# Performance work log

Measured on AMD Instinct MI355X. Metric: run time of the kernel, lower is better.

Reference implementation:

```python
import jax, jax.numpy as jnp
import numpy as np

NUM_CLASSES = 80
MASK_SIZE = 3
ATTRIBS = 5 + NUM_CLASSES
NET_W = 608.0
NET_H = 608.0
# Faithful to the original indexing bug: anchor_w = masked_anchors[a], anchor_h = masked_anchors[a+1]
MASKED_ANCHORS = np.array([10.0, 13.0, 16.0, 30.0, 33.0, 23.0], dtype=np.float32)
ANCHOR_W = jnp.asarray(MASKED_ANCHORS[0:MASK_SIZE])      # [10, 13, 16]
ANCHOR_H = jnp.asarray(MASKED_ANCHORS[1:MASK_SIZE + 1])  # [13, 16, 30]


def setup_inputs() -> dict:
    key = jax.random.key(0)
    x = jax.random.normal(key, (16, MASK_SIZE * ATTRIBS, 76, 76), dtype=jnp.float32)
    return {"x": x}


def reference(x):
    B, C, H, W = x.shape
    # (B, A, attribs, H, W) -> (B, A, H, W, attribs)
    pred = x.reshape(B, MASK_SIZE, ATTRIBS, H, W).transpose(0, 1, 3, 4, 2)
    tx = jax.nn.sigmoid(pred[..., 0])
    ty = jax.nn.sigmoid(pred[..., 1])
    tw = pred[..., 2]
    th = pred[..., 3]
    conf = jax.nn.sigmoid(pred[..., 4])
    pred_cls = jax.nn.sigmoid(pred[..., 5:])

    gi = jnp.arange(W, dtype=x.dtype)[None, None, None, :]  # column index i
    gj = jnp.arange(H, dtype=x.dtype)[None, None, :, None]  # row index j
    bx = (gi + tx) / W
    by = (gj + ty) / H
    bw = jnp.exp(tw) * ANCHOR_W[None, :, None, None] / NET_W
    bh = jnp.exp(th) * ANCHOR_H[None, :, None, None] / NET_H

    boxes = jnp.stack([bx, by, bw, bh], axis=-1)  # (B, A, H, W, 4)
    # (B, A, H, W, 4+1+num_classes)
    return jnp.concatenate([boxes, conf[..., None], pred_cls], axis=-1)
```

## Files before the change

### kernel.cpp

```cpp
#include <hip/hip_runtime.h>
#include <stdint.h>

#define NB      16
#define NA      3
#define HH_     76
#define WW_     76
#define S_TOT   (HH_ * WW_)
#define ATTR    85
#define TILE_S  76
#define TILES   (S_TOT / TILE_S)
#define CHUNKS4 (TILE_S / 4)
#define UNITS_L (ATTR * CHUNKS4)
#define UNITS_S (TILE_S * ATTR / 4)
#define NTHREADS 256
#define LOG2E   1.44269504088896340f

typedef __attribute__((ext_vector_type(4))) float float4v;

__device__ __forceinline__ float fast_sigmoid(float x) {
    float e = __builtin_amdgcn_exp2f(x * (-LOG2E));
    return __builtin_amdgcn_rcpf(1.0f + e);
}

__global__ __launch_bounds__(NTHREADS)
void yolo_layer_kernel(const float* __restrict__ in,
                       float* __restrict__ out) {
    __shared__ __attribute__((aligned(16))) float lds[TILE_S * ATTR];

    const int tid  = threadIdx.x;
    const int tile = blockIdx.x;
    const int BA   = blockIdx.y;
    const int a    = BA % NA;
    const int s0   = tile * TILE_S;

    const float aw = (a == 0) ? 10.0f : (a == 1) ? 13.0f : 16.0f;
    const float ah = (a == 0) ? 13.0f : (a == 1) ? 16.0f : 30.0f;
    const float cw = aw * (1.0f / 608.0f);
    const float ch = ah * (1.0f / 608.0f);

    const float* inb = in + (size_t)BA * (ATTR * S_TOT) + s0;

    for (int u = tid; u < UNITS_L; u += NTHREADS) {
        const int k  = u / CHUNKS4;
        const int c  = u - k * CHUNKS4;
        const int sl = c * 4;

        const float4v v = *(const float4v*)(inb + (size_t)k * S_TOT + sl);
        float r[4];

        if (k >= 4) {
            #pragma unroll
            for (int j = 0; j < 4; ++j) {
                r[j] = fast_sigmoid(v[j]);
            }
        } else {
            #pragma unroll
            for (int j = 0; j < 4; ++j) {
                float x  = v[j];
                int   sp = s0 + sl + j;
                int   hy = sp / WW_;
                int   wx = sp - hy * WW_;
                if      (k == 0) r[j] = ((float)wx + fast_sigmoid(x)) * (1.0f / 76.0f);
                else if (k == 1) r[j] = ((float)hy + fast_sigmoid(x)) * (1.0f / 76.0f);
                else if (k == 2) r[j] = __builtin_amdgcn_exp2f(x * LOG2E) * cw;
                else             r[j] = __builtin_amdgcn_exp2f(x * LOG2E) * ch;
            }
        }

        float* lp = &lds[sl * ATTR + k];
        #pragma unroll
        for (int j = 0; j < 4; ++j) {
            lp[j * ATTR] = r[j];
        }
    }

    __syncthreads();

    float4v* outv = (float4v*)(out + ((size_t)BA * S_TOT + s0) * ATTR);
    const float4v* ldsv = (const float4v*)lds;
    for (int u = tid; u < UNITS_S; u += NTHREADS) {
        outv[u] = ldsv[u];
    }
}

extern "C" void kernel_launch(void* const* d_in, const int* in_sizes, int n_in,
                              void* d_out, int out_size, void* d_ws, size_t ws_size,
                              hipStream_t stream) {
    const float* in = (const float*)d_in[0];
    float* out = (float*)d_out;

    dim3 grid(TILES, NB * NA);
    dim3 block(NTHREADS);
    yolo_layer_kernel<<<grid, block, 0, stream>>>(in, out);
}
```

Baseline: 168.8 us.

## Give each wave a private 16-position tile with all loads issued upfront

Each wavefront now owns its own 16-position spatial micro-tile and its own LDS slice. The block-wide __syncthreads is gone, and the grid becomes one-dimensional over all micro-tiles. Every lane issues six float4 loads before doing any math, which raises memory-level parallelism, and output goes out through nontemporal stores with a launch-bounds occupancy hint. The cost is shorter contiguous input reads (64 bytes per attribute row instead of 304). A few lanes also do redundant clamped loads and rewrite the same values to the last attribute row.

```diff
diff --git a/kernel.cpp b/kernel.cpp
--- a/kernel.cpp
+++ b/kernel.cpp
@@ -3,15 +3,12 @@
 
 #define NB      16
 #define NA      3
-#define HH_     76
-#define WW_     76
-#define S_TOT   (HH_ * WW_)
+#define S_TOT   5776
 #define ATTR    85
-#define TILE_S  76
-#define TILES   (S_TOT / TILE_S)
-#define CHUNKS4 (TILE_S / 4)
-#define UNITS_L (ATTR * CHUNKS4)
-#define UNITS_S (TILE_S * ATTR / 4)
+#define MT_S    16
+#define MT_PER  361
+#define N_MT    (NB * NA * MT_PER)
+#define WPB     4
 #define NTHREADS 256
 #define LOG2E   1.44269504088896340f
 
@@ -22,64 +19,73 @@
     return __builtin_amdgcn_rcpf(1.0f + e);
 }
 
-__global__ __launch_bounds__(NTHREADS)
+__global__ __launch_bounds__(NTHREADS, 7)
 void yolo_layer_kernel(const float* __restrict__ in,
                        float* __restrict__ out) {
-    __shared__ __attribute__((aligned(16))) float lds[TILE_S * ATTR];
+    __shared__ __attribute__((aligned(16))) float lds[WPB * MT_S * ATTR];
 
-    const int tid  = threadIdx.x;
-    const int tile = blockIdx.x;
-    const int BA   = blockIdx.y;
+    const int lane = threadIdx.x & 63;
+    const int wave = threadIdx.x >> 6;
+    const int g    = blockIdx.x * WPB + wave;
+    const int BA   = g / MT_PER;
+    const int m    = g - BA * MT_PER;
     const int a    = BA % NA;
-    const int s0   = tile * TILE_S;
+    const int s0   = m * MT_S;
 
     const float aw = (a == 0) ? 10.0f : (a == 1) ? 13.0f : 16.0f;
     const float ah = (a == 0) ? 13.0f : (a == 1) ? 16.0f : 30.0f;
     const float cw = aw * (1.0f / 608.0f);
     const float ch = ah * (1.0f / 608.0f);
 
+    float* L = lds + wave * (MT_S * ATTR);
     const float* inb = in + (size_t)BA * (ATTR * S_TOT) + s0;
 
-    for (int u = tid; u < UNITS_L; u += NTHREADS) {
-        const int k  = u / CHUNKS4;
-        const int c  = u - k * CHUNKS4;
-        const int sl = c * 4;
+    const int c  = lane & 3;
+    const int kb = lane >> 2;
+    float4v v[6];
+    #pragma unroll
+    for (int i = 0; i < 6; ++i) {
+        int kk = kb + 16 * i;
+        kk = (kk > 84) ? 84 : kk;
+        v[i] = *(const float4v*)(inb + (size_t)kk * S_TOT + c * 4);
+    }
 
-        const float4v v = *(const float4v*)(inb + (size_t)k * S_TOT + sl);
+    #pragma unroll
+    for (int i = 0; i < 6; ++i) {
+        int kk = kb + 16 * i;
+        kk = (kk > 84) ? 84 : kk;
+
         float r[4];
-
-        if (k >= 4) {
+        if (kk >= 4) {
             #pragma unroll
-            for (int j = 0; j < 4; ++j) {
-                r[j] = fast_sigmoid(v[j]);
-            }
+            for (int j = 0; j < 4; ++j) r[j] = fast_sigmoid(v[i][j]);
         } else {
             #pragma unroll
             for (int j = 0; j < 4; ++j) {
-                float x  = v[j];
-                int   sp = s0 + sl + j;
-                int   hy = sp / WW_;
-                int   wx = sp - hy * WW_;
-                if      (k == 0) r[j] = ((float)wx + fast_sigmoid(x)) * (1.0f / 76.0f);
-                else if (k == 1) r[j] = ((float)hy + fast_sigmoid(x)) * (1.0f / 76.0f);
-                else if (k == 2) r[j] = __builtin_amdgcn_exp2f(x * LOG2E) * cw;
-                else             r[j] = __builtin_amdgcn_exp2f(x * LOG2E) * ch;
+                float x  = v[i][j];
+                int   sp = s0 + c * 4 + j;
+                int   hy = sp / 76;
+                int   wx = sp - hy * 76;
+                if      (kk == 0) r[j] = ((float)wx + fast_sigmoid(x)) * (1.0f / 76.0f);
+                else if (kk == 1) r[j] = ((float)hy + fast_sigmoid(x)) * (1.0f / 76.0f);
+                else if (kk == 2) r[j] = __builtin_amdgcn_exp2f(x * LOG2E) * cw;
+                else              r[j] = __builtin_amdgcn_exp2f(x * LOG2E) * ch;
             }
         }
 
-        float* lp = &lds[sl * ATTR + k];
+        float* lp = &L[c * 4 * ATTR + kk];
         #pragma unroll
-        for (int j = 0; j < 4; ++j) {
-            lp[j * ATTR] = r[j];
-        }
+        for (int j = 0; j < 4; ++j) lp[j * ATTR] = r[j];
     }
 
-    __syncthreads();
-
     float4v* outv = (float4v*)(out + ((size_t)BA * S_TOT + s0) * ATTR);
-    const float4v* ldsv = (const float4v*)lds;
-    for (int u = tid; u < UNITS_S; u += NTHREADS) {
-        outv[u] = ldsv[u];
+    const float4v* Lv = (const float4v*)L;
+    #pragma unroll
+    for (int i = 0; i < 6; ++i) {
+        int idx = lane + 64 * i;
+        if (idx < MT_S * ATTR / 4) {
+            __builtin_nontemporal_store(Lv[idx], &outv[idx]);
+        }
     }
 }
 
@@ -89,7 +95,7 @@
     const float* in = (const float*)d_in[0];
     float* out = (float*)d_out;
 
-    dim3 grid(TILES, NB * NA);
+    dim3 grid(N_MT / WPB);
     dim3 block(NTHREADS);
     yolo_layer_kernel<<<grid, block, 0, stream>>>(in, out);
 }
```

Measured after the change: 165.2 us. 2.1% less time.
